# Kernel tuning notes

Measured on AMD Instinct MI355X. Metric: run time of the kernel, lower is better.

Reference implementation:

```python
import jax, jax.numpy as jnp
import numpy as np

NUM_EMBEDDING = 8192
EMBEDDING_DIM = 512
BS = 16384
NEG_SLOPE = 0.01  # torch LeakyReLU default


def setup_inputs() -> dict:
    key = jax.random.key(0)
    k1, k2, k3, k4, k5, k6, k7 = jax.random.split(key, 7)
    d, K = EMBEDDING_DIM, NUM_EMBEDDING
    s1 = 1.0 / np.sqrt(d)
    return {
        "encoded_eeg": jax.random.normal(k1, (BS, d), dtype=jnp.float32),
        "encoded_mel": jax.random.normal(k2, (BS, d), dtype=jnp.float32),
        "embeddings": jax.random.normal(k3, (K, d), dtype=jnp.float32),
        "W1": jax.random.uniform(k4, (d, d), jnp.float32, -s1, s1),
        "b1": jax.random.uniform(k5, (d,), jnp.float32, -s1, s1),
        "W2": jax.random.uniform(k6, (K, d), jnp.float32, -s1, s1),
        "b2": jax.random.uniform(k7, (K,), jnp.float32, -s1, s1),
    }


def reference(encoded_eeg, encoded_mel, embeddings, W1, b1, W2, b2):
    # --- nearest-codebook indices for mel (detached in original) ---
    flat_mel = encoded_mel.reshape(-1, EMBEDDING_DIM)
    dists = (jnp.sum(embeddings ** 2, axis=1)[None, :]
             + jnp.sum(flat_mel ** 2, axis=1, keepdims=True)
             - 2.0 * flat_mel @ embeddings.T)  # [BS, K]
    mel_indices = jnp.argmin(dists, axis=-1)  # [BS]

    # --- small MLP logits over eeg ---
    flat_eeg = encoded_eeg.reshape(-1, EMBEDDING_DIM)
    h = flat_eeg @ W1.T + b1
    h = jnp.where(h >= 0, h, NEG_SLOPE * h)  # LeakyReLU
    logits = h @ W2.T + b2  # [BS, K]

    eeg_indices = jnp.argmax(logits, axis=-1)
    acc_rate = jnp.mean((eeg_indices == mel_indices).astype(jnp.float32))

    # cross entropy (mean over batch)
    logp = jax.nn.log_softmax(logits, axis=-1)
    loss = -jnp.mean(jnp.take_along_axis(logp, mel_indices[:, None], axis=1))
    return (loss, acc_rate)
```

## Files before the change

### kernel.cpp

```cpp
#include <hip/hip_runtime.h>
#include <hip/hip_bf16.h>
#include <hip/hip_fp8.h>

#define BSZ 16384
#define DIM 512
#define NEMB 8192
#define NEG 0.01f
#define NSPLIT 8

typedef __attribute__((ext_vector_type(8))) short short8;
typedef __attribute__((ext_vector_type(4))) float f32x4;
typedef __attribute__((ext_vector_type(4))) int i32x4;
typedef __attribute__((ext_vector_type(8))) int i32x8;

typedef const __attribute__((address_space(1))) void GVT;
typedef __attribute__((address_space(3))) void LVT;

__device__ __forceinline__ void gl_lds16(const void* g, void* l) {
    __builtin_amdgcn_global_load_lds((GVT*)g, (LVT*)l, 16, 0, 0);
}

__device__ __forceinline__ float bf2f(unsigned short u) {
    union { unsigned int i; float f; } c; c.i = ((unsigned int)u) << 16; return c.f;
}
__device__ __forceinline__ unsigned short f2bf(float f) {
    union { __hip_bfloat16 h; unsigned short u; } c; c.h = __float2bfloat16(f); return c.u;
}
__device__ __forceinline__ unsigned char f2fp8(float f) {
    __hip_fp8_e4m3 t(f); return (unsigned char)t.__x;
}
__device__ __forceinline__ unsigned int fkey(float f) {
    unsigned int u = __float_as_uint(f);
    return u ^ ((unsigned int)((int)u >> 31) | 0x80000000u);
}

__device__ __forceinline__ size_t pack_addr(int r, int k) {
    int kg = k >> 6, ko = k & 63;
    int half = ko >> 5, lq = (ko & 31) >> 3, sub = ko & 7;
    int L = lq * 16 + (r & 15);
    return ((size_t)((r >> 4) * 8 + kg) << 10) + (size_t)(L << 4) + (half << 3) + sub;
}

__device__ __forceinline__ void vm4_barrier() {
    asm volatile("s_waitcnt vmcnt(4) lgkmcnt(0)\ns_barrier" ::: "memory");
}
__device__ __forceinline__ void vm0_barrier() {
    asm volatile("s_waitcnt vmcnt(0) lgkmcnt(0)\ns_barrier" ::: "memory");
}
__device__ __forceinline__ void lgkm_barrier() {
    asm volatile("s_waitcnt lgkmcnt(0)\ns_barrier" ::: "memory");
}

#define ISSUE_NT(NT, BUF) do { \
    const unsigned char* src_ = gB0p + (size_t)(NT) * 16384; \
    _Pragma("unroll") for (int i_ = 0; i_ < 4; i_++) \
        gl_lds16(src_ + i_ * 1024, &sB8[BUF][uWd + i_ * 1024]); \
} while (0)

#define LOADH(F0, F1, CUR, KP) do { \
    const unsigned char* lb_ = &sB8[CUR][(2 * (KP)) * 1024] + (lane << 4); \
    i32x4 a0_ = *(const i32x4*)lb_; \
    i32x4 a1_ = *(const i32x4*)(lb_ + 1024); \
    i32x4 b0_ = *(const i32x4*)(lb_ + 8192); \
    i32x4 b1_ = *(const i32x4*)(lb_ + 8192 + 1024); \
    F0 = __builtin_shufflevector(a0_, a1_, 0, 1, 2, 3, 4, 5, 6, 7); \
    F1 = __builtin_shufflevector(b0_, b1_, 0, 1, 2, 3, 4, 5, 6, 7); \
} while (0)

#define MFMA4(F0, F1, KP, FIRST) do { \
    __builtin_amdgcn_s_setprio(1); \
    _Pragma("unroll") for (int mi = 0; mi < 2; mi++) { \
        f32x4 c0_ = (FIRST) ? Z4 : acc[mi][0]; \
        f32x4 c1_ = (FIRST) ? Z4 : acc[mi][1]; \
        acc[mi][0] = __builtin_amdgcn_mfma_scale_f32_16x16x128_f8f6f4( \
            fa8[mi][KP], F0, c0_, 0, 0, 0, 0x7F7F7F7Fu, 0, 0x7F7F7F7Fu); \
        acc[mi][1] = __builtin_amdgcn_mfma_scale_f32_16x16x128_f8f6f4( \
            fa8[mi][KP], F1, c1_, 0, 0, 0, 0x7F7F7F7Fu, 0, 0x7F7F7F7Fu); \
    } \
    __builtin_amdgcn_s_setprio(0); \
} while (0)

#define COMPUTE(CUR) do { \
    LOADH(fA0, fA1, CUR, 0); \
    LOADH(fB0, fB1, CUR, 1); \
    MFMA4(fA0, fA1, 0, 1); \
    LOADH(fA0, fA1, CUR, 2); \
    MFMA4(fB0, fB1, 1, 0); \
    LOADH(fB0, fB1, CUR, 3); \
    MFMA4(fA0, fA1, 2, 0); \
    MFMA4(fB0, fB1, 3, 0); \
} while (0)

#define EPILOGUE(NT) do { \
    int j0 = ((NT) << 5) + l15; \
    if (is_logits) { \
        float bb0 = sAux[j0], bb1 = sAux[j0 + 16]; \
        unsigned int ic0 = (unsigned int)(NEMB - 1 - (nbase + j0)); \
        _Pragma("unroll") for (int mi = 0; mi < 2; mi++) \
            _Pragma("unroll") for (int rg = 0; rg < 4; rg++) { \
                float v0 = acc[mi][0][rg] + bb0; \
                float v1 = acc[mi][1][rg] + bb1; \
                int r = mi * 4 + rg; \
                s[r] += __expf(v0) + __expf(v1); \
                float m = fmaxf(v0, v1); \
                unsigned int ii = v1 > v0 ? ic0 - 16 : ic0; \
                unsigned int pk = (fkey(m) & 0xFFFFE000u) | ii; \
                pbest[r] = pbest[r] > pk ? pbest[r] : pk; \
            } \
    } else { \
        float en0 = sAux[j0], en1 = sAux[j0 + 16]; \
        unsigned int cl0 = (unsigned int)(nbase + j0); \
        _Pragma("unroll") for (int mi = 0; mi < 2; mi++) \
            _Pragma("unroll") for (int rg = 0; rg < 4; rg++) { \
                float v0 = fmaf(-2.f, acc[mi][0][rg], en0); \
                float v1 = fmaf(-2.f, acc[mi][1][rg], en1); \
                float m = fminf(v0, v1); \
                unsigned int ii = v1 < v0 ? cl0 + 16 : cl0; \
                unsigned int pk = (fkey(m) & 0xFFFFE000u) | ii; \
                int r = mi * 4 + rg; \
                pbest[r] = pbest[r] < pk ? pbest[r] : pk; \
            } \
    } \
} while (0)

__global__ void k_prep(const float* __restrict__ eeg, const float* __restrict__ mel,
                       const float* __restrict__ emb, const float* __restrict__ W2,
                       const float* __restrict__ W1,
                       unsigned short* __restrict__ o_eeg, unsigned short* __restrict__ o_w1,
                       unsigned char* __restrict__ o_mel8, unsigned char* __restrict__ o_emb8,
                       unsigned char* __restrict__ o_w28,
                       float* __restrict__ enorm,
                       float* __restrict__ acc2, int* __restrict__ cnt) {
    __shared__ float sps[4];
    int bid = blockIdx.x, tid = threadIdx.x;
    int w = tid >> 6, lane = tid & 63;
    if (bid == 0 && tid == 0) { acc2[0] = 0.f; acc2[1] = 0.f; *cnt = 0; }
    const int n_big = BSZ * DIM / 4;
    const int n_mid = NEMB * DIM / 4;
    const int n_w1  = DIM * DIM / 4;
    const int total = n_big * 2 + n_mid * 2 + n_w1;
    for (int i = bid * 256 + tid; i < total; i += 1024 * 256) {
        int j = i;
        if (j < n_big) {
            float4 v = ((const float4*)eeg)[j];
            ushort4 o; o.x = f2bf(v.x); o.y = f2bf(v.y); o.z = f2bf(v.z); o.w = f2bf(v.w);
            ((ushort4*)o_eeg)[j] = o;
        } else if ((j -= n_big) < n_w1) {
            float4 v = ((const float4*)W1)[j];
            ushort4 o; o.x = f2bf(v.x); o.y = f2bf(v.y); o.z = f2bf(v.z); o.w = f2bf(v.w);
            ((ushort4*)o_w1)[j] = o;
        } else if ((j -= n_w1) < n_big) {
            float4 v = ((const float4*)mel)[j];
            uchar4 o; o.x = f2fp8(v.x); o.y = f2fp8(v.y); o.z = f2fp8(v.z); o.w = f2fp8(v.w);
            *(uchar4*)(o_mel8 + pack_addr(j >> 7, (j & 127) * 4)) = o;
        } else if ((j -= n_big) < n_mid) {
            float4 v = ((const float4*)emb)[j];
            uchar4 o; o.x = f2fp8(v.x); o.y = f2fp8(v.y); o.z = f2fp8(v.z); o.w = f2fp8(v.w);
            *(uchar4*)(o_emb8 + pack_addr(j >> 7, (j & 127) * 4)) = o;
            float ss = v.x*v.x + v.y*v.y + v.z*v.z + v.w*v.w;
            #pragma unroll
            for (int d = 1; d < 64; d <<= 1) ss += __shfl_xor(ss, d);
            if (lane == 0) sps[w] = ss;
            __syncthreads();
            if (tid == 0)   enorm[j >> 7]       = sps[0] + sps[1];
            if (tid == 128) enorm[(j >> 7)]     = sps[2] + sps[3];
            __syncthreads();
        } else {
            j -= n_mid;
            float4 v = ((const float4*)W2)[j];
            uchar4 o; o.x = f2fp8(v.x); o.y = f2fp8(v.y); o.z = f2fp8(v.z); o.w = f2fp8(v.w);
            *(uchar4*)(o_w28 + pack_addr(j >> 7, (j & 127) * 4)) = o;
        }
    }
}

__launch_bounds__(256, 2)
__global__ void k_hgemm(const unsigned short* __restrict__ A,
                        const unsigned short* __restrict__ B,
                        const float* __restrict__ b1,
                        unsigned short* __restrict__ H,
                        unsigned char* __restrict__ H8) {
    __shared__ __align__(16) unsigned short sA[4096], sB[4096];
    int tid = threadIdx.x;
    int w = tid >> 6, lane = tid & 63;
    int wr = w >> 1, wc = w & 1;
    int lquad = lane >> 4, l15 = lane & 15;
    int mt = blockIdx.x >> 2, nt = blockIdx.x & 3;
    int m0 = mt * 128, n0 = nt * 128;

    int e0 = w * 512 + lane * 8;
    int r0 = e0 >> 5, ce = e0 & 31;
    const unsigned short* gA0 = A + (m0 + r0) * DIM + ce;
    const unsigned short* gA1 = gA0 + 64 * DIM;
    const unsigned short* gB0 = B + (n0 + r0) * DIM + ce;
    const unsigned short* gB1 = gB0 + 64 * DIM;
    unsigned short* lA0 = sA + w * 512;  unsigned short* lA1 = sA + (w + 4) * 512;
    unsigned short* lB0 = sB + w * 512;  unsigned short* lB1 = sB + (w + 4) * 512;

    int offA[4], offB[4];
    #pragma unroll
    for (int i = 0; i < 4; i++) {
        offA[i] = (wr * 64 + i * 16 + l15) * 32 + lquad * 8;
        offB[i] = (wc * 64 + i * 16 + l15) * 32 + lquad * 8;
    }

    f32x4 acc[4][4];
    #pragma unroll
    for (int mi = 0; mi < 4; mi++)
        #pragma unroll
        for (int ni = 0; ni < 4; ni++) acc[mi][ni] = 0;

    for (int kk = 0; kk < 16; kk++) {
        gl_lds16(gA0, lA0); gl_lds16(gA1, lA1);
        gl_lds16(gB0, lB0); gl_lds16(gB1, lB1);
        gA0 += 32; gA1 += 32; gB0 += 32; gB1 += 32;
        __syncthreads();
        short8 af[4], bf_[4];
        #pragma unroll
        for (int i = 0; i < 4; i++) {
            af[i]  = *(const short8*)&sA[offA[i]];
            bf_[i] = *(const short8*)&sB[offB[i]];
        }
        #pragma unroll
        for (int mi = 0; mi < 4; mi++)
            #pragma unroll
            for (int ni = 0; ni < 4; ni++)
                acc[mi][ni] = __builtin_amdgcn_mfma_f32_16x16x32_bf16(af[mi], bf_[ni], acc[mi][ni], 0, 0, 0);
        __syncthreads();
    }

    #pragma unroll
    for (int ni = 0; ni < 4; ni++) {
        int col = n0 + wc * 64 + ni * 16 + l15;
        float bv = b1[col];
        #pragma unroll
        for (int mi = 0; mi < 4; mi++) {
            int rowb = m0 + wr * 64 + mi * 16 + lquad * 4;
            #pragma unroll
            for (int rg = 0; rg < 4; rg++) {
                float v = acc[mi][ni][rg] + bv;
                v = v >= 0.f ? v : NEG * v;
                H[(rowb + rg) * DIM + col] = f2bf(v);
                H8[pack_addr(rowb + rg, col)] = f2fp8(v);
            }
        }
    }
}

__launch_bounds__(256, 3)
__global__ void k_big(const unsigned char* __restrict__ Mel8,
                      const unsigned char* __restrict__ Emb8,
                      const unsigned char* __restrict__ H8,
                      const unsigned char* __restrict__ W28,
                      const float* __restrict__ enorm,
                      const float* __restrict__ b2,
                      float* __restrict__ p_s,
                      unsigned int* __restrict__ p_pmax,
                      unsigned int* __restrict__ p_pmin) {
    __shared__ __align__(16) unsigned char sB8[2][16384];
    __shared__ float sAux[1024];
    int tid = threadIdx.x;
    int w = tid >> 6, lane = tid & 63;
    int lquad = lane >> 4, l15 = lane & 15;
    int bid = blockIdx.x;
    int split = bid & 7;
    int is_logits = (bid >> 3) & 1;
    int mt = bid >> 4;
    int m0 = mt * 128, nbase = split * (NEMB / NSPLIT);

    const unsigned char* gAb = (is_logits ? H8 : Mel8);
    const unsigned char* gBb = (is_logits ? W28 : Emb8);

    #pragma unroll
    for (int j = 0; j < 4; j++) {
        int c = tid + j * 256;
        sAux[c] = is_logits ? b2[nbase + c] : (enorm[nbase + c] - 512.0f);
    }

    i32x8 fa8[2][4];
    #pragma unroll
    for (int mi = 0; mi < 2; mi++)
        #pragma unroll
        for (int kp = 0; kp < 4; kp++) {
            const unsigned char* p = gAb
                + ((size_t)(((m0 >> 4) + 2 * w + mi) * 8 + 2 * kp) << 10) + lane * 16;
            i32x4 lo = *(const i32x4*)p;
            i32x4 hi = *(const i32x4*)(p + 1024);
            fa8[mi][kp] = __builtin_shufflevector(lo, hi, 0, 1, 2, 3, 4, 5, 6, 7);
        }

    int uWd = w * 4096;
    const unsigned char* gB0p = gBb + (size_t)nbase * 512 + uWd + lane * 16;

    __syncthreads();

    const f32x4 Z4 = {0.f, 0.f, 0.f, 0.f};
    f32x4 acc[2][2];
    i32x8 fA0, fA1, fB0, fB1;

    float s[8];
    unsigned int pbest[8];
    unsigned int pinit = is_logits ? 0u : 0xFFFFFFFFu;
    #pragma unroll
    for (int r = 0; r < 8; r++) { s[r] = 0.f; pbest[r] = pinit; }

    ISSUE_NT(0, 0);
    ISSUE_NT(1, 1);
    for (int nt = 0; nt < 32; nt++) {
        int cur = nt & 1;
        if (nt < 31) vm4_barrier(); else vm0_barrier();
        COMPUTE(cur);
        lgkm_barrier();
        if (nt + 2 < 32) ISSUE_NT(nt + 2, cur);
        EPILOGUE(nt);
    }

    if (is_logits) {
        #pragma unroll
        for (int r = 0; r < 8; r++)
            #pragma unroll
            for (int d = 1; d < 16; d <<= 1) {
                s[r] += __shfl_xor(s[r], d);
                unsigned int o = (unsigned int)__shfl_xor((int)pbest[r], d);
                pbest[r] = pbest[r] > o ? pbest[r] : o;
            }
        if (l15 == 0) {
            #pragma unroll
            for (int mi = 0; mi < 2; mi++)
                #pragma unroll
                for (int rg = 0; rg < 4; rg++) {
                    int row = w * 32 + mi * 16 + lquad * 4 + rg;
                    int pidx = split * BSZ + m0 + row;
                    p_s[pidx] = s[mi * 4 + rg];
                    p_pmax[pidx] = pbest[mi * 4 + rg];
                }
        }
    } else {
        #pragma unroll
        for (int r = 0; r < 8; r++)
            #pragma unroll
            for (int d = 1; d < 16; d <<= 1) {
                unsigned int o = (unsigned int)__shfl_xor((int)pbest[r], d);
                pbest[r] = pbest[r] < o ? pbest[r] : o;
            }
        if (l15 == 0) {
            #pragma unroll
            for (int mi = 0; mi < 2; mi++)
                #pragma unroll
                for (int rg = 0; rg < 4; rg++) {
                    int row = w * 32 + mi * 16 + lquad * 4 + rg;
                    p_pmin[split * BSZ + m0 + row] = pbest[mi * 4 + rg];
                }
        }
    }
}

__global__ void k_tail(const float* __restrict__ p_s, const unsigned int* __restrict__ p_pmax,
                       const unsigned int* __restrict__ p_pmin,
                       const unsigned short* __restrict__ H,
                       const float* __restrict__ W2,
                       const float* __restrict__ b2,
                       float* __restrict__ acc2, int* __restrict__ cnt,
                       float* __restrict__ out) {
    __shared__ int s_idx[64];
    __shared__ float s_l1[64], s_match[64];
    __shared__ float s_d[4];
    int bid = blockIdx.x, tid = threadIdx.x;
    int w = tid >> 6, lane = tid & 63;
    int rbase = bid * 64;

    if (tid < 64) {
        int r = rbase + tid;
        float S = 0.f; unsigned int PM = 0u, PN = 0xFFFFFFFFu;
        #pragma unroll
        for (int sp = 0; sp < NSPLIT; sp++) {
            S += p_s[sp * BSZ + r];
            unsigned int a = p_pmax[sp * BSZ + r];
            PM = PM > a ? PM : a;
            unsigned int b = p_pmin[sp * BSZ + r];
            PN = PN < b ? PN : b;
        }
        int eidx = (NEMB - 1) - (int)(PM & 0x1FFFu);
        int midx = (int)(PN & 0x1FFFu);
        s_idx[tid] = midx;
        s_l1[tid] = __logf(S) - b2[midx];
        s_match[tid] = (eidx == midx) ? 1.f : 0.f;
    }
    __syncthreads();

    float d0 = 0.f, d1 = 0.f;
    for (int j = 0; j < 16; j++) {
        int rr = w * 16 + j;
        int ridx = s_idx[rr];
        uint4 hv = *(const uint4*)(H + (size_t)(rbase + rr) * DIM + lane * 8);
        const float4* wp = (const float4*)(W2 + (size_t)ridx * DIM + lane * 8);
        float4 w0 = wp[0], w1 = wp[1];
        float p = bf2f((unsigned short)(hv.x & 0xffff)) * w0.x + bf2f((unsigned short)(hv.x >> 16)) * w0.y
                + bf2f((unsigned short)(hv.y & 0xffff)) * w0.z + bf2f((unsigned short)(hv.y >> 16)) * w0.w
                + bf2f((unsigned short)(hv.z & 0xffff)) * w1.x + bf2f((unsigned short)(hv.z >> 16)) * w1.y
                + bf2f((unsigned short)(hv.w & 0xffff)) * w1.z + bf2f((unsigned short)(hv.w >> 16)) * w1.w;
        if (j & 1) d1 += p; else d0 += p;
    }
    float ds = d0 + d1;
    #pragma unroll
    for (int d = 1; d < 64; d <<= 1) ds += __shfl_xor(ds, d);
    if (lane == 0) s_d[w] = ds;

    __syncthreads();
    for (int st = 32; st > 0; st >>= 1) {
        if (tid < st) { s_l1[tid] += s_l1[tid + st]; s_match[tid] += s_match[tid + st]; }
        __syncthreads();
    }
    if (tid == 0) {
        float loss_blk = s_l1[0] - (s_d[0] + s_d[1] + s_d[2] + s_d[3]);
        atomicAdd(&acc2[0], loss_blk * (1.0f / BSZ));
        atomicAdd(&acc2[1], s_match[0] * (1.0f / BSZ));
        __threadfence();
        if (atomicAdd(cnt, 1) == 255) {
            float L = atomicAdd(&acc2[0], 0.f);
            float M = atomicAdd(&acc2[1], 0.f);
            out[0] = L; out[1] = M;
        }
    }
}

extern "C" void kernel_launch(void* const* d_in, const int* in_sizes, int n_in,
                              void* d_out, int out_size, void* d_ws, size_t ws_size,
                              hipStream_t stream) {
    const float* eeg = (const float*)d_in[0];
    const float* mel = (const float*)d_in[1];
    const float* emb = (const float*)d_in[2];
    const float* W1  = (const float*)d_in[3];
    const float* b1  = (const float*)d_in[4];
    const float* W2  = (const float*)d_in[5];
    const float* b2  = (const float*)d_in[6];
    float* out = (float*)d_out;

    unsigned short* ws_eeg = (unsigned short*)d_ws;
    unsigned short* ws_w1  = ws_eeg + (size_t)BSZ * DIM;
    unsigned short* ws_h   = ws_w1  + (size_t)DIM * DIM;
    unsigned char*  ws_h8  = (unsigned char*)(ws_h + (size_t)BSZ * DIM);
    unsigned char*  ws_mel8 = ws_h8  + (size_t)BSZ * DIM;
    unsigned char*  ws_emb8 = ws_mel8 + (size_t)BSZ * DIM;
    unsigned char*  ws_w28  = ws_emb8 + (size_t)NEMB * DIM;
    float* ws_en  = (float*)(ws_w28 + (size_t)NEMB * DIM);
    float* p_s    = ws_en + NEMB;
    unsigned int* p_pmax = (unsigned int*)(p_s + (size_t)NSPLIT * BSZ);
    unsigned int* p_pmin = p_pmax + (size_t)NSPLIT * BSZ;
    float* acc2   = (float*)(p_pmin + (size_t)NSPLIT * BSZ);
    int*   cnt    = (int*)(acc2 + 2);

    k_prep<<<1024, 256, 0, stream>>>(eeg, mel, emb, W2, W1,
                                     ws_eeg, ws_w1, ws_mel8, ws_emb8, ws_w28,
                                     ws_en, acc2, cnt);
    k_hgemm<<<(BSZ / 128) * (DIM / 128), 256, 0, stream>>>(ws_eeg, ws_w1, b1, ws_h, ws_h8);
    k_big<<<(BSZ / 128) * NSPLIT * 2, 256, 0, stream>>>(ws_mel8, ws_emb8, ws_h8, ws_w28,
                                                        ws_en, b2, p_s, p_pmax, p_pmin);
    k_tail<<<BSZ / 64, 256, 0, stream>>>(p_s, p_pmax, p_pmin, ws_h, W2, b2, acc2, cnt, out);
}
```

Before: 325.8 us.

## Split prep kernel by role, write packed fp8 tiles whole, retile hidden GEMM

The prep kernel now gives separate block ranges to the bf16 conversion, the fp8 packing and the embedding-norm computation. This drops the per-iteration __syncthreads and the scattered 4-byte packed stores in favour of one 16-byte store per lane of a packed tile. The hidden-layer GEMM moves to 64-row tiles with a 64-wide K step (two sub-slabs per barrier) and allows 4 blocks per CU, which doubles the grid and halves the barrier count. The risk is that the packed-fp8 index mapping must match the old pack_addr layout exactly, and the smaller M tile reloads the B (W1) tile more often.

```diff
diff --git a/kernel.cpp b/kernel.cpp
--- a/kernel.cpp
+++ b/kernel.cpp
@@ -131,101 +131,111 @@
                        unsigned char* __restrict__ o_w28,
                        float* __restrict__ enorm,
                        float* __restrict__ acc2, int* __restrict__ cnt) {
-    __shared__ float sps[4];
     int bid = blockIdx.x, tid = threadIdx.x;
     int w = tid >> 6, lane = tid & 63;
     if (bid == 0 && tid == 0) { acc2[0] = 0.f; acc2[1] = 0.f; *cnt = 0; }
-    const int n_big = BSZ * DIM / 4;
-    const int n_mid = NEMB * DIM / 4;
-    const int n_w1  = DIM * DIM / 4;
-    const int total = n_big * 2 + n_mid * 2 + n_w1;
-    for (int i = bid * 256 + tid; i < total; i += 1024 * 256) {
-        int j = i;
-        if (j < n_big) {
-            float4 v = ((const float4*)eeg)[j];
-            ushort4 o; o.x = f2bf(v.x); o.y = f2bf(v.y); o.z = f2bf(v.z); o.w = f2bf(v.w);
-            ((ushort4*)o_eeg)[j] = o;
-        } else if ((j -= n_big) < n_w1) {
-            float4 v = ((const float4*)W1)[j];
-            ushort4 o; o.x = f2bf(v.x); o.y = f2bf(v.y); o.z = f2bf(v.z); o.w = f2bf(v.w);
-            ((ushort4*)o_w1)[j] = o;
-        } else if ((j -= n_w1) < n_big) {
-            float4 v = ((const float4*)mel)[j];
-            uchar4 o; o.x = f2fp8(v.x); o.y = f2fp8(v.y); o.z = f2fp8(v.z); o.w = f2fp8(v.w);
-            *(uchar4*)(o_mel8 + pack_addr(j >> 7, (j & 127) * 4)) = o;
-        } else if ((j -= n_big) < n_mid) {
-            float4 v = ((const float4*)emb)[j];
-            uchar4 o; o.x = f2fp8(v.x); o.y = f2fp8(v.y); o.z = f2fp8(v.z); o.w = f2fp8(v.w);
-            *(uchar4*)(o_emb8 + pack_addr(j >> 7, (j & 127) * 4)) = o;
-            float ss = v.x*v.x + v.y*v.y + v.z*v.z + v.w*v.w;
-            #pragma unroll
-            for (int d = 1; d < 64; d <<= 1) ss += __shfl_xor(ss, d);
-            if (lane == 0) sps[w] = ss;
-            __syncthreads();
-            if (tid == 0)   enorm[j >> 7]       = sps[0] + sps[1];
-            if (tid == 128) enorm[(j >> 7)]     = sps[2] + sps[3];
-            __syncthreads();
-        } else {
-            j -= n_mid;
-            float4 v = ((const float4*)W2)[j];
-            uchar4 o; o.x = f2fp8(v.x); o.y = f2fp8(v.y); o.z = f2fp8(v.z); o.w = f2fp8(v.w);
-            *(uchar4*)(o_w28 + pack_addr(j >> 7, (j & 127) * 4)) = o;
-        }
-    }
-}
-
-__launch_bounds__(256, 2)
+    if (bid < 512) {
+        const int n_big = BSZ * DIM / 4;
+        const int n_w1  = DIM * DIM / 4;
+        const int total = n_big + n_w1;
+        for (int i = bid * 256 + tid; i < total; i += 512 * 256) {
+            if (i < n_big) {
+                float4 v = ((const float4*)eeg)[i];
+                ushort4 o; o.x = f2bf(v.x); o.y = f2bf(v.y); o.z = f2bf(v.z); o.w = f2bf(v.w);
+                ((ushort4*)o_eeg)[i] = o;
+            } else {
+                int j = i - n_big;
+                float4 v = ((const float4*)W1)[j];
+                ushort4 o; o.x = f2bf(v.x); o.y = f2bf(v.y); o.z = f2bf(v.z); o.w = f2bf(v.w);
+                ((ushort4*)o_w1)[j] = o;
+            }
+        }
+    } else if (bid < 896) {
+        int wid = (bid - 512) * 4 + w;
+        for (int u = wid; u < 16384; u += 384 * 4) {
+            const float* src; unsigned char* dst; int lu;
+            if (u < 8192)       { src = mel; dst = o_mel8; lu = u; }
+            else if (u < 12288) { src = emb; dst = o_emb8; lu = u - 8192; }
+            else                { src = W2;  dst = o_w28;  lu = u - 12288; }
+            int r  = ((lu >> 3) << 4) + (lane & 15);
+            int kg = lu & 7;
+            int f4 = r * 128 + kg * 16 + (lane >> 4) * 2;
+            float4 f0 = ((const float4*)src)[f4];
+            float4 f1 = ((const float4*)src)[f4 + 1];
+            float4 f2 = ((const float4*)src)[f4 + 8];
+            float4 f3 = ((const float4*)src)[f4 + 9];
+            union { unsigned char b[16]; uint4 v; } o;
+            o.b[0]  = f2fp8(f0.x); o.b[1]  = f2fp8(f0.y); o.b[2]  = f2fp8(f0.z); o.b[3]  = f2fp8(f0.w);
+            o.b[4]  = f2fp8(f1.x); o.b[5]  = f2fp8(f1.y); o.b[6]  = f2fp8(f1.z); o.b[7]  = f2fp8(f1.w);
+            o.b[8]  = f2fp8(f2.x); o.b[9]  = f2fp8(f2.y); o.b[10] = f2fp8(f2.z); o.b[11] = f2fp8(f2.w);
+            o.b[12] = f2fp8(f3.x); o.b[13] = f2fp8(f3.y); o.b[14] = f2fp8(f3.z); o.b[15] = f2fp8(f3.w);
+            *(uint4*)(dst + (size_t)lu * 1024 + lane * 16) = o.v;
+        }
+    } else {
+        int wid = (bid - 896) * 4 + w;
+        for (int row = wid; row < NEMB; row += 128 * 4) {
+            const float4* p = (const float4*)(emb + (size_t)row * DIM) + lane * 2;
+            float4 a = p[0], b = p[1];
+            float s = a.x*a.x + a.y*a.y + a.z*a.z + a.w*a.w
+                    + b.x*b.x + b.y*b.y + b.z*b.z + b.w*b.w;
+            #pragma unroll
+            for (int d = 1; d < 64; d <<= 1) s += __shfl_xor(s, d);
+            if (lane == 0) enorm[row] = s;
+        }
+    }
+}
+
+__launch_bounds__(256, 4)
 __global__ void k_hgemm(const unsigned short* __restrict__ A,
                         const unsigned short* __restrict__ B,
                         const float* __restrict__ b1,
                         unsigned short* __restrict__ H,
                         unsigned char* __restrict__ H8) {
-    __shared__ __align__(16) unsigned short sA[4096], sB[4096];
+    __shared__ __align__(16) unsigned short sA[2][2048], sB[2][4096];
     int tid = threadIdx.x;
     int w = tid >> 6, lane = tid & 63;
     int wr = w >> 1, wc = w & 1;
     int lquad = lane >> 4, l15 = lane & 15;
     int mt = blockIdx.x >> 2, nt = blockIdx.x & 3;
-    int m0 = mt * 128, n0 = nt * 128;
-
-    int e0 = w * 512 + lane * 8;
-    int r0 = e0 >> 5, ce = e0 & 31;
-    const unsigned short* gA0 = A + (m0 + r0) * DIM + ce;
-    const unsigned short* gA1 = gA0 + 64 * DIM;
-    const unsigned short* gB0 = B + (n0 + r0) * DIM + ce;
-    const unsigned short* gB1 = gB0 + 64 * DIM;
-    unsigned short* lA0 = sA + w * 512;  unsigned short* lA1 = sA + (w + 4) * 512;
-    unsigned short* lB0 = sB + w * 512;  unsigned short* lB1 = sB + (w + 4) * 512;
-
-    int offA[4], offB[4];
-    #pragma unroll
-    for (int i = 0; i < 4; i++) {
-        offA[i] = (wr * 64 + i * 16 + l15) * 32 + lquad * 8;
-        offB[i] = (wc * 64 + i * 16 + l15) * 32 + lquad * 8;
-    }
-
-    f32x4 acc[4][4];
-    #pragma unroll
-    for (int mi = 0; mi < 4; mi++)
+    int m0 = mt * 64, n0 = nt * 128;
+
+    int e2 = w * 512 + lane * 8;
+    int rA = e2 >> 5, cA = e2 & 31;
+
+    int offA[2], offB[4];
+    #pragma unroll
+    for (int i = 0; i < 2; i++) offA[i] = (wr * 32 + i * 16 + l15) * 32 + lquad * 8;
+    #pragma unroll
+    for (int i = 0; i < 4; i++) offB[i] = (wc * 64 + i * 16 + l15) * 32 + lquad * 8;
+
+    f32x4 acc[2][4];
+    #pragma unroll
+    for (int mi = 0; mi < 2; mi++)
         #pragma unroll
         for (int ni = 0; ni < 4; ni++) acc[mi][ni] = 0;
 
-    for (int kk = 0; kk < 16; kk++) {
-        gl_lds16(gA0, lA0); gl_lds16(gA1, lA1);
-        gl_lds16(gB0, lB0); gl_lds16(gB1, lB1);
-        gA0 += 32; gA1 += 32; gB0 += 32; gB1 += 32;
+    for (int kk = 0; kk < 8; kk++) {
+        int kb = kk * 64;
+        gl_lds16(A + (size_t)(m0 + rA) * DIM + kb + cA,        &sA[0][e2]);
+        gl_lds16(A + (size_t)(m0 + rA) * DIM + kb + 32 + cA,   &sA[1][e2]);
+        gl_lds16(B + (size_t)(n0 + rA) * DIM + kb + cA,        &sB[0][e2]);
+        gl_lds16(B + (size_t)(n0 + rA + 64) * DIM + kb + cA,   &sB[0][e2 + 2048]);
+        gl_lds16(B + (size_t)(n0 + rA) * DIM + kb + 32 + cA,   &sB[1][e2]);
+        gl_lds16(B + (size_t)(n0 + rA + 64) * DIM + kb + 32 + cA, &sB[1][e2 + 2048]);
         __syncthreads();
-        short8 af[4], bf_[4];
-        #pragma unroll
-        for (int i = 0; i < 4; i++) {
-            af[i]  = *(const short8*)&sA[offA[i]];
-            bf_[i] = *(const short8*)&sB[offB[i]];
-        }
-        #pragma unroll
-        for (int mi = 0; mi < 4; mi++)
-            #pragma unroll
-            for (int ni = 0; ni < 4; ni++)
-                acc[mi][ni] = __builtin_amdgcn_mfma_f32_16x16x32_bf16(af[mi], bf_[ni], acc[mi][ni], 0, 0, 0);
+        #pragma unroll
+        for (int ks = 0; ks < 2; ks++) {
+            short8 af[2], bf_[4];
+            #pragma unroll
+            for (int i = 0; i < 2; i++) af[i]  = *(const short8*)&sA[ks][offA[i]];
+            #pragma unroll
+            for (int i = 0; i < 4; i++) bf_[i] = *(const short8*)&sB[ks][offB[i]];
+            #pragma unroll
+            for (int mi = 0; mi < 2; mi++)
+                #pragma unroll
+                for (int ni = 0; ni < 4; ni++)
+                    acc[mi][ni] = __builtin_amdgcn_mfma_f32_16x16x32_bf16(af[mi], bf_[ni], acc[mi][ni], 0, 0, 0);
+        }
         __syncthreads();
     }
 
@@ -234,13 +244,13 @@
         int col = n0 + wc * 64 + ni * 16 + l15;
         float bv = b1[col];
         #pragma unroll
-        for (int mi = 0; mi < 4; mi++) {
-            int rowb = m0 + wr * 64 + mi * 16 + lquad * 4;
+        for (int mi = 0; mi < 2; mi++) {
+            int rowb = m0 + wr * 32 + mi * 16 + lquad * 4;
             #pragma unroll
             for (int rg = 0; rg < 4; rg++) {
                 float v = acc[mi][ni][rg] + bv;
                 v = v >= 0.f ? v : NEG * v;
-                H[(rowb + rg) * DIM + col] = f2bf(v);
+                H[(size_t)(rowb + rg) * DIM + col] = f2bf(v);
                 H8[pack_addr(rowb + rg, col)] = f2fp8(v);
             }
         }
@@ -453,7 +463,7 @@
     k_prep<<<1024, 256, 0, stream>>>(eeg, mel, emb, W2, W1,
                                      ws_eeg, ws_w1, ws_mel8, ws_emb8, ws_w28,
                                      ws_en, acc2, cnt);
-    k_hgemm<<<(BSZ / 128) * (DIM / 128), 256, 0, stream>>>(ws_eeg, ws_w1, b1, ws_h, ws_h8);
+    k_hgemm<<<(BSZ / 64) * (DIM / 128), 256, 0, stream>>>(ws_eeg, ws_w1, b1, ws_h, ws_h8);
     k_big<<<(BSZ / 128) * NSPLIT * 2, 256, 0, stream>>>(ws_mel8, ws_emb8, ws_h8, ws_w28,
                                                         ws_en, b2, p_s, p_pmax, p_pmin);
     k_tail<<<BSZ / 64, 256, 0, stream>>>(p_s, p_pmax, p_pmin, ws_h, W2, b2, acc2, cnt, out);
```

New measurement: 325.4 us. About the same (-0.1%).
